# Kernel tuning notes

Hardware: AMD Instinct MI355X
Metric: run time of the kernel (lower is better)

The kernel has to match this reference:

```python
import jax, jax.numpy as jnp
import numpy as np


def _layernorm(x, g, b, eps=1e-5):
    m = x.mean(-1, keepdims=True)
    v = ((x - m) ** 2).mean(-1, keepdims=True)
    return (x - m) * jax.lax.rsqrt(v + eps) * g + b


def setup_inputs() -> dict:
    key = jax.random.key(0)
    ks = jax.random.split(key, 12)
    B, V, E, N = 8, 64, 512, 32          # batch, num_vars, embed(=input_dim), num_samples
    L, H, D, M, R = 4, 8, 64, 1024, 128  # layers, heads, head_dim, mlp_dim, resolution
    HD = H * D
    s = 0.02
    return {
        "flow_encoded": jax.random.normal(ks[0], (B, V, E), jnp.float32),
        "W_shift": s * jax.random.normal(ks[1], (E, HD), jnp.float32),
        "b_shift": jnp.zeros((HD,), jnp.float32),
        "Wk": s * jax.random.normal(ks[2], (L, H, E, D), jnp.float32),
        "bk": jnp.zeros((L, H, D), jnp.float32),
        "Wv": s * jax.random.normal(ks[3], (L, H, E, D), jnp.float32),
        "bv": jnp.zeros((L, H, D), jnp.float32),
        "ln1_g": jnp.ones((L, HD), jnp.float32),
        "ln1_b": jnp.zeros((L, HD), jnp.float32),
        "W1": s * jax.random.normal(ks[4], (L, HD, M), jnp.float32),
        "b1": jnp.zeros((L, M), jnp.float32),
        "W2": s * jax.random.normal(ks[5], (L, M, M), jnp.float32),
        "b2": jnp.zeros((L, M), jnp.float32),
        "W3": s * jax.random.normal(ks[6], (L, M, HD), jnp.float32),
        "b3": jnp.zeros((L, HD), jnp.float32),
        "ln2_g": jnp.ones((L, HD), jnp.float32),
        "ln2_b": jnp.zeros((L, HD), jnp.float32),
        "W_dist": s * jax.random.normal(ks[7], (HD, R), jnp.float32),
        "b_dist": jnp.zeros((R,), jnp.float32),
        "num_samples": N,
    }


def _forward_logits(flow_encoded, W_shift, b_shift, Wk, bk, Wv, bv,
                    ln1_g, ln1_b, W1, b1, W2, b2, W3, b3, ln2_g, ln2_b,
                    W_dist, b_dist, num_samples):
    B, V, E = flow_encoded.shape
    L, H, _, D = Wk.shape
    HD = H * D
    # history keys/values: all heads in one einsum (replaces per-head nn.Linear loop)
    keys = jnp.einsum('bve,lhed->lbhvd', flow_encoded, Wk) + bk[:, None, :, None, :]
    vals = jnp.einsum('bve,lhed->lbhvd', flow_encoded, Wv) + bv[:, None, :, None, :]
    # queries per (var, sample); vectorized over vars (outer loop in source is independent)
    att = flow_encoded @ W_shift + b_shift                      # [B, V, HD]
    att = jnp.broadcast_to(att[:, :, None, :], (B, V, num_samples, HD))
    scale = D ** -0.5
    for l in range(L):
        q = att.reshape(B, V, num_samples, H, D)
        scores = jnp.einsum('bvnhd,bhwd->bvnhw', q, keys[l]) * scale
        w = jax.nn.softmax(scores, axis=-1)
        a = jnp.einsum('bvnhw,bhwd->bvnhd', w, vals[l]).reshape(B, V, num_samples, HD)
        att = _layernorm(att + a, ln1_g[l], ln1_b[l])
        h = jax.nn.relu(att @ W1[l] + b1[l])
        h = jax.nn.relu(h @ W2[l] + b2[l])
        h = h @ W3[l] + b3[l]
        att = _layernorm(att + h, ln2_g[l], ln2_b[l])
    return att @ W_dist + b_dist                                # [B, V, N, R]


def reference(flow_encoded, W_shift, b_shift, Wk, bk, Wv, bv,
              ln1_g, ln1_b, W1, b1, W2, b2, W3, b3, ln2_g, ln2_b,
              W_dist, b_dist, num_samples):
    logits = _forward_logits(flow_encoded, W_shift, b_shift, Wk, bk, Wv, bv,
                             ln1_g, ln1_b, W1, b1, W2, b2, W3, b3, ln2_g, ln2_b,
                             W_dist, b_dist, num_samples)
    R = b_dist.shape[0]
    k = jax.random.key(1)
    idx = jax.random.categorical(jax.random.fold_in(k, 0), logits, axis=-1)  # multinomial(1)
    u = jax.random.uniform(jax.random.fold_in(k, 1), idx.shape, jnp.float32)
    samples = (idx.astype(jnp.float32) + u) / R                 # [B, V, N]
    return samples
```

## Files before the change

### kernel.cpp

```cpp
#include <hip/hip_runtime.h>
#include <hip/hip_bf16.h>
#include <math.h>

constexpr int B  = 8,  V = 64, E = 512, NS = 32;
constexpr int L  = 4,  H = 8,  D = 64,  M  = 1024, R = 128;
constexpr int HD = H * D;
constexpr int ROWS  = B * V;
constexpr int SROWS = ROWS * NS;
constexpr int KVN = 4096;

typedef _Float16 half8 __attribute__((ext_vector_type(8)));
typedef float floatx4 __attribute__((ext_vector_type(4)));

struct TF2 { unsigned a, b; };
__host__ __device__ constexpr unsigned rotl32(unsigned x, int d) {
  return (x << d) | (x >> (32 - d));
}
__host__ __device__ constexpr TF2 threefry(unsigned k0, unsigned k1,
                                           unsigned x0, unsigned x1) {
  unsigned ks2 = k0 ^ k1 ^ 0x1BD11BDAu;
  x0 += k0; x1 += k1;
  const int ra[4] = {13, 15, 26, 6};
  const int rb[4] = {17, 29, 16, 24};
  for (int i = 0; i < 4; i++) { x0 += x1; x1 = rotl32(x1, ra[i]); x1 ^= x0; }
  x0 += k1;  x1 += ks2 + 1u;
  for (int i = 0; i < 4; i++) { x0 += x1; x1 = rotl32(x1, rb[i]); x1 ^= x0; }
  x0 += ks2; x1 += k0 + 2u;
  for (int i = 0; i < 4; i++) { x0 += x1; x1 = rotl32(x1, ra[i]); x1 ^= x0; }
  x0 += k0;  x1 += k1 + 3u;
  for (int i = 0; i < 4; i++) { x0 += x1; x1 = rotl32(x1, rb[i]); x1 ^= x0; }
  x0 += k1;  x1 += ks2 + 4u;
  for (int i = 0; i < 4; i++) { x0 += x1; x1 = rotl32(x1, ra[i]); x1 ^= x0; }
  x0 += ks2; x1 += k0 + 5u;
  return {x0, x1};
}
__device__ __forceinline__ unsigned tf_bits32(unsigned k0, unsigned k1,
                                              unsigned j) {
  TF2 r = threefry(k0, k1, 0u, j);
  return r.a ^ r.b;
}

__device__ __forceinline__ double waveReduceAdd64(double v) {
#pragma unroll
  for (int m = 32; m; m >>= 1) v += __shfl_xor(v, m, 64);
  return v;
}

__device__ __forceinline__ void split16(float v, _Float16& h, _Float16& l) {
  h = (_Float16)v;
  l = (_Float16)((v - (float)h) * 2048.0f);
}

struct WArgs {
  const float* s[7];
  _Float16* h[7];
  _Float16* l[7];
};
__global__ __launch_bounds__(256) void prep_split(
    WArgs a, const float* __restrict__ flow, const float* __restrict__ bk,
    const float* __restrict__ bv, const float* __restrict__ bsh,
    _Float16* __restrict__ fh, _Float16* __restrict__ fl,
    float* __restrict__ kvb, float* __restrict__ logits) {
  __shared__ float tile[64][65];
  const int bid = blockIdx.x, t = threadIdx.x;
  if (bid < 275) {
    if (bid < 256) {
      const int base = (bid * 256 + t) * 4;
      float4 v = *(const float4*)&flow[base];
      float x[4] = {v.x, v.y, v.z, v.w};
#pragma unroll
      for (int j = 0; j < 4; j++) {
        _Float16 h, l;
        split16(x[j], h, l);
        fh[base + j] = h;
        fl[base + j] = l;
      }
    } else {
      const int idx = (bid - 256) * 256 + t;
      if (idx < KVN + HD) {
        float bb = (idx < 2048) ? bk[idx]
                 : (idx < 4096) ? bv[idx - 2048]
                                : bsh[idx - 4096];
        kvb[idx] = bb;
      }
    }
    return;
  }
  if (bid >= 2915) {
    const int idx = (bid - 2915) * 256 + t;
    float4 z = {0.f, 0.f, 0.f, 0.f};
    *(float4*)&logits[idx * 4] = z;
    return;
  }
  const int WS_OFF[8] = {0, 64, 320, 576, 1088, 2112, 2624, 2640};
  const int WS_K[7] = {512, 512, 512, 512, 1024, 1024, 512};
  const int WS_N[7] = {512, 64, 64, 1024, 1024, 512, 128};
  int wb = bid - 275;
  int mi = 0;
  while (wb >= WS_OFF[mi + 1]) mi++;
  int tt = wb - WS_OFF[mi];
  const int K = WS_K[mi], N = WS_N[mi];
  const int ktiles = K >> 6;
  const int per = ktiles * (N >> 6);
  const int z = tt / per;
  const int rem = tt - z * per;
  const int k0 = (rem % ktiles) * 64, n0 = (rem / ktiles) * 64;
  const size_t moff = (size_t)z * K * N;
  const float* src = a.s[mi] + moff;
  _Float16* dh = a.h[mi] + moff;
  _Float16* dl = a.l[mi] + moff;
#pragma unroll
  for (int i = 0; i < 16; i++) {
    int idx = i * 256 + t, r = idx >> 6, c = idx & 63;
    tile[r][c] = src[(size_t)(k0 + r) * N + n0 + c];
  }
  __syncthreads();
#pragma unroll
  for (int i = 0; i < 16; i++) {
    int idx = i * 256 + t, n = idx >> 6, k = idx & 63;
    float v = tile[k][n];
    _Float16 h, l;
    split16(v, h, l);
    dh[(size_t)(n0 + n) * K + k0 + k] = h;
    dl[(size_t)(n0 + n) * K + k0 + k] = l;
  }
}

#define GEMM64_BODY(Ah, Al, Bh, Bl, K, m0, n0, kbase, kchunk, hh, mid, lds)  \
  {                                                                          \
    const int t = threadIdx.x, lane = t & 63, wave = t >> 6;                 \
    const int KT = (kchunk) >> 5;                                            \
    const int l15w = lane & 15, quadw = lane >> 4;                           \
    const _Float16* srcs[4] = {                                              \
        (Ah) + (size_t)(m0) * (K), (Al) + (size_t)(m0) * (K),                \
        (Bh) + (size_t)(n0) * (K), (Bl) + (size_t)(n0) * (K)};               \
    const _Float16* gsrc =                                                   \
        srcs[wave] + (size_t)l15w * (K) + quadw * 8 + (kbase);               \
    auto stage = [&](int buf, int kt) {                                      \
      _Float16* base = &lds[buf * 8192 + wave * 2048];                       \
      const int koff = kt * 32;                                              \
      _Pragma("unroll") for (int f = 0; f < 4; f++)                          \
          __builtin_amdgcn_global_load_lds(                                  \
              gsrc + (size_t)(f * 16) * (K) + koff, base + f * 512, 16, 0,   \
              0);                                                            \
    };                                                                       \
    const int wm = wave >> 1, wn = wave & 1;                                 \
    stage(0, 0);                                                             \
    __syncthreads();                                                         \
    for (int kt = 0; kt < KT; kt++) {                                        \
      if (kt + 1 < KT) stage((kt + 1) & 1, kt + 1);                          \
      const int bofs = (kt & 1) * 8192;                                      \
      half8 a_h[2], a_l[2], b_h[2], b_l[2];                                  \
      _Pragma("unroll") for (int i = 0; i < 2; i++) {                        \
        const int af = (wm * 2 + i) * 512 + lane * 8;                        \
        const int bf = (wn * 2 + i) * 512 + lane * 8;                        \
        a_h[i] = *(const half8*)&lds[bofs + af];                             \
        a_l[i] = *(const half8*)&lds[bofs + 2048 + af];                      \
        b_h[i] = *(const half8*)&lds[bofs + 4096 + bf];                      \
        b_l[i] = *(const half8*)&lds[bofs + 6144 + bf];                      \
      }                                                                      \
      _Pragma("unroll") for (int i = 0; i < 2; i++)                          \
          _Pragma("unroll") for (int j = 0; j < 2; j++) {                    \
        hh[i][j] = __builtin_amdgcn_mfma_f32_16x16x32_f16(a_h[i], b_h[j],    \
                                                          hh[i][j], 0, 0, 0);\
        mid[i][j] = __builtin_amdgcn_mfma_f32_16x16x32_f16(                  \
            a_h[i], b_l[j], mid[i][j], 0, 0, 0);                             \
        mid[i][j] = __builtin_amdgcn_mfma_f32_16x16x32_f16(                  \
            a_l[i], b_h[j], mid[i][j], 0, 0, 0);                             \
      }                                                                      \
      __syncthreads();                                                       \
    }                                                                        \
  }

#define GEMM_ACC_INIT(hh, mid)                                               \
  floatx4 hh[2][2], mid[2][2];                                               \
  _Pragma("unroll") for (int i = 0; i < 2; i++)                              \
      _Pragma("unroll") for (int j = 0; j < 2; j++) {                        \
    hh[i][j] = (floatx4){0.f, 0.f, 0.f, 0.f};                                \
    mid[i][j] = (floatx4){0.f, 0.f, 0.f, 0.f};                               \
  }

__global__ __launch_bounds__(256) void gemm_kv(
    const _Float16* __restrict__ Ah, const _Float16* __restrict__ Al,
    const _Float16* __restrict__ Bh, const _Float16* __restrict__ Bl,
    const float* __restrict__ kvb, float* __restrict__ kv,
    float* __restrict__ att) {
  __shared__ __align__(16) _Float16 lds[2 * 8192];
  const int n0 = blockIdx.x * 64, m0 = blockIdx.y * 64;
  GEMM_ACC_INIT(hh, mid)
  GEMM64_BODY(Ah, Al, Bh, Bl, 512, m0, n0, 0, 512, hh, mid, lds)
  const int t = threadIdx.x, lane = t & 63, wave = t >> 6;
  const int wm = wave >> 1, wn = wave & 1, quad = lane >> 4, l15 = lane & 15;
#pragma unroll
  for (int i = 0; i < 2; i++)
#pragma unroll
    for (int j = 0; j < 2; j++)
#pragma unroll
      for (int r = 0; r < 4; r++) {
        float v = hh[i][j][r] + mid[i][j][r] * (1.0f / 2048.0f);
        const int m = m0 + (wm * 2 + i) * 16 + quad * 4 + r;
        const int n = n0 + (wn * 2 + j) * 16 + l15;
        v += kvb[n];
        if (n < KVN) kv[(size_t)m * KVN + n] = v;
        else att[(size_t)m * HD + (n - KVN)] = v;
      }
}

__global__ __launch_bounds__(256) void gemm_sp(
    const _Float16* __restrict__ Ah, const _Float16* __restrict__ Al,
    const _Float16* __restrict__ Bh, const _Float16* __restrict__ Bl,
    float* __restrict__ P, int K, int kchunk, int Ndim) {
  __shared__ __align__(16) _Float16 lds[2 * 8192];
  const int n0 = blockIdx.x * 64, m0 = blockIdx.y * 64;
  const int kbase = blockIdx.z * kchunk;
  GEMM_ACC_INIT(hh, mid)
  GEMM64_BODY(Ah, Al, Bh, Bl, K, m0, n0, kbase, kchunk, hh, mid, lds)
  const int t = threadIdx.x, lane = t & 63, wave = t >> 6;
  const int wm = wave >> 1, wn = wave & 1, quad = lane >> 4, l15 = lane & 15;
  float* Pz = P + (size_t)blockIdx.z * ROWS * Ndim;
#pragma unroll
  for (int i = 0; i < 2; i++)
#pragma unroll
    for (int j = 0; j < 2; j++)
#pragma unroll
      for (int r = 0; r < 4; r++) {
        float v = hh[i][j][r] + mid[i][j][r] * (1.0f / 2048.0f);
        const int m = m0 + (wm * 2 + i) * 16 + quad * 4 + r;
        const int n = n0 + (wn * 2 + j) * 16 + l15;
        Pz[(size_t)m * Ndim + n] = v;
      }
}

__global__ __launch_bounds__(256) void gemm_dist(
    const _Float16* __restrict__ Ah, const _Float16* __restrict__ Al,
    const _Float16* __restrict__ Bh, const _Float16* __restrict__ Bl,
    const float* __restrict__ bd, float* __restrict__ logits) {
  __shared__ __align__(16) _Float16 lds[2 * 8192];
  const int n0 = blockIdx.x * 64, m0 = blockIdx.y * 64;
  const int kbase = blockIdx.z * 256;
  GEMM_ACC_INIT(hh, mid)
  GEMM64_BODY(Ah, Al, Bh, Bl, 512, m0, n0, kbase, 256, hh, mid, lds)
  const int t = threadIdx.x, lane = t & 63, wave = t >> 6;
  const int wm = wave >> 1, wn = wave & 1, quad = lane >> 4, l15 = lane & 15;
#pragma unroll
  for (int i = 0; i < 2; i++)
#pragma unroll
    for (int j = 0; j < 2; j++)
#pragma unroll
      for (int r = 0; r < 4; r++) {
        float v = hh[i][j][r] + mid[i][j][r] * (1.0f / 2048.0f);
        const int m = m0 + (wm * 2 + i) * 16 + quad * 4 + r;
        const int n = n0 + (wn * 2 + j) * 16 + l15;
        if (blockIdx.z == 0) v += bd[n];
        atomicAdd(&logits[(size_t)m * R + n], v);
      }
}

__global__ __launch_bounds__(256) void epi_h(
    const float* __restrict__ P, const float* __restrict__ bias,
    _Float16* __restrict__ Oh, _Float16* __restrict__ Ol, int Ndim, int kz,
    int relu) {
  const int n = blockIdx.x * 256 + threadIdx.x;
  const int m = blockIdx.y;
  const size_t MN = (size_t)ROWS * Ndim;
  const size_t id = (size_t)m * Ndim + n;
  float v = 0.0f;
  for (int z = 0; z < kz; z++) v += P[z * MN + id];
  v += bias[n];
  if (relu) v = fmaxf(v, 0.0f);
  _Float16 h, l;
  split16(v, h, l);
  Oh[id] = h;
  Ol[id] = l;
}

__device__ __forceinline__ void attn_core(
    float* __restrict__ att, _Float16* __restrict__ att_h,
    _Float16* __restrict__ att_l, const float* __restrict__ kv,
    const float* __restrict__ g, const float* __restrict__ bb, int l, int row,
    float q0, float q1) {
  __shared__ float q[HD];
  __shared__ float sp[HD];
  __shared__ double rb[8];
  const int t = threadIdx.x;
  const int b_ = row >> 6;
  q[t] = q0;
  q[t + 256] = q1;
  __syncthreads();
#pragma unroll
  for (int rep = 0; rep < 2; rep++) {
    int idx = t + rep * 256;
    int h = idx >> 6, w = idx & 63;
    const float* kp = kv + (size_t)(b_ * 64 + w) * KVN + (l * 8 + h) * 64;
    const float* qp = q + h * D;
    double s = 0.0;
#pragma unroll 8
    for (int d = 0; d < 64; d++) s += (double)qp[d] * (double)kp[d];
    sp[idx] = (float)s * 0.125f;
  }
  __syncthreads();
  {
    int h = t >> 5, w0 = t & 31;
    float s0 = sp[h * 64 + w0], s1 = sp[h * 64 + w0 + 32];
    float mx = fmaxf(s0, s1);
#pragma unroll
    for (int m = 16; m; m >>= 1) mx = fmaxf(mx, __shfl_xor(mx, m, 32));
    float e0 = expf(s0 - mx), e1 = expf(s1 - mx);
    double sm = (double)e0 + (double)e1;
#pragma unroll
    for (int m = 16; m; m >>= 1) sm += __shfl_xor(sm, m, 32);
    sp[h * 64 + w0]      = (float)((double)e0 / sm);
    sp[h * 64 + w0 + 32] = (float)((double)e1 / sm);
  }
  __syncthreads();
  float x[2];
#pragma unroll
  for (int rep = 0; rep < 2; rep++) {
    int idx = t + rep * 256;
    int h = idx >> 6, d = idx & 63;
    const float* vp =
        kv + (size_t)(b_ * 64) * KVN + 2048 + (l * 8 + h) * 64 + d;
    const float* pp = sp + h * 64;
    double acc = 0.0;
#pragma unroll 8
    for (int w = 0; w < 64; w++)
      acc += (double)pp[w] * (double)vp[(size_t)w * KVN];
    x[rep] = q[idx] + (float)acc;
  }
  double s1 = (double)x[0] + (double)x[1];
  double s2 = (double)x[0] * (double)x[0] + (double)x[1] * (double)x[1];
  s1 = waveReduceAdd64(s1);
  s2 = waveReduceAdd64(s2);
  const int wid = t >> 6, lane = t & 63;
  if (lane == 0) { rb[wid] = s1; rb[4 + wid] = s2; }
  __syncthreads();
  double S1 = rb[0] + rb[1] + rb[2] + rb[3];
  double S2 = rb[4] + rb[5] + rb[6] + rb[7];
  double mean = S1 / (double)HD;
  double var  = S2 / (double)HD - mean * mean;
  double inv  = 1.0 / sqrt(var + (double)1e-5f);
  float y0 =
      (float)(((double)x[0] - mean) * inv * (double)g[t] + (double)bb[t]);
  float y1 = (float)(((double)x[1] - mean) * inv * (double)g[t + 256] +
                     (double)bb[t + 256]);
  att[row * HD + t] = y0;
  att[row * HD + 256 + t] = y1;
  _Float16 h0, l0, h1v, l1v;
  split16(y0, h0, l0);
  split16(y1, h1v, l1v);
  att_h[row * HD + t] = h0;
  att_l[row * HD + t] = l0;
  att_h[row * HD + 256 + t] = h1v;
  att_l[row * HD + 256 + t] = l1v;
}

__global__ __launch_bounds__(256) void attn_kernel(
    float* __restrict__ att, _Float16* __restrict__ att_h,
    _Float16* __restrict__ att_l, const float* __restrict__ kv,
    const float* __restrict__ g, const float* __restrict__ bb, int l) {
  const int t = threadIdx.x, row = blockIdx.x;
  float q0 = att[row * HD + t];
  float q1 = att[row * HD + 256 + t];
  attn_core(att, att_h, att_l, kv, g, bb, l, row, q0, q1);
}

__global__ __launch_bounds__(256) void epi_ln_attn(
    float* __restrict__ att, _Float16* __restrict__ att_h,
    _Float16* __restrict__ att_l, const float* __restrict__ P,
    const float* __restrict__ b3, const float* __restrict__ g2,
    const float* __restrict__ bb2, const float* __restrict__ kv,
    const float* __restrict__ g1, const float* __restrict__ bb1, int next_l) {
  __shared__ double rb[8];
  const int t = threadIdx.x, row = blockIdx.x;
  const size_t MN = (size_t)ROWS * HD;
  const size_t id0 = (size_t)row * HD + t;
  float h0 = 0.0f, h1s = 0.0f;
  for (int z = 0; z < 8; z++) {
    h0 += P[z * MN + id0];
    h1s += P[z * MN + id0 + 256];
  }
  h0 += b3[t];
  h1s += b3[t + 256];
  float x0 = att[id0] + h0;
  float x1 = att[id0 + 256] + h1s;
  double s1 = (double)x0 + (double)x1;
  double s2 = (double)x0 * (double)x0 + (double)x1 * (double)x1;
  s1 = waveReduceAdd64(s1);
  s2 = waveReduceAdd64(s2);
  const int wid = t >> 6, lane = t & 63;
  if (lane == 0) { rb[wid] = s1; rb[4 + wid] = s2; }
  __syncthreads();
  double S1 = rb[0] + rb[1] + rb[2] + rb[3];
  double S2 = rb[4] + rb[5] + rb[6] + rb[7];
  double mean = S1 / (double)HD;
  double var  = S2 / (double)HD - mean * mean;
  double inv  = 1.0 / sqrt(var + (double)1e-5f);
  float y0 =
      (float)(((double)x0 - mean) * inv * (double)g2[t] + (double)bb2[t]);
  float y1 = (float)(((double)x1 - mean) * inv * (double)g2[t + 256] +
                     (double)bb2[t + 256]);
  if (next_l < 0) {
    att[id0] = y0;
    att[id0 + 256] = y1;
    _Float16 hh0, ll0, hh1, ll1;
    split16(y0, hh0, ll0);
    split16(y1, hh1, ll1);
    att_h[id0] = hh0;
    att_l[id0] = ll0;
    att_h[id0 + 256] = hh1;
    att_l[id0 + 256] = ll1;
  } else {
    __syncthreads();
    attn_core(att, att_h, att_l, kv, g1, bb1, next_l, row, y0, y1);
  }
}

__global__ __launch_bounds__(256) void sample_kernel(
    const float* __restrict__ logits, float* __restrict__ out) {
  constexpr TF2 KC = threefry(0u, 1u, 0u, 0u);
  constexpr TF2 KU = threefry(0u, 1u, 0u, 1u);
  const int lane = threadIdx.x & 63;
  const int wid = threadIdx.x >> 6;
  const int row = blockIdx.x * 4 + wid;
  const float* lrow = logits + (row >> 5) * R;
  float bvv = -1e30f;
  int bi = 0;
#pragma unroll
  for (int rep = 0; rep < 2; rep++) {
    int r = lane + rep * 64;
    unsigned j = (unsigned)row * (unsigned)R + (unsigned)r;
    unsigned bits = tf_bits32(KC.a, KC.b, j);
    float f = __uint_as_float((bits >> 9) | 0x3f800000u) - 1.0f;
    float u = fmaxf(f, 1.17549435e-38f);
    float gv = -logf(-logf(u));
    float v = lrow[r] + gv;
    if (v > bvv) { bvv = v; bi = r; }
  }
#pragma unroll
  for (int m = 32; m; m >>= 1) {
    float ov = __shfl_xor(bvv, m, 64);
    int oi = __shfl_xor(bi, m, 64);
    if (ov > bvv || (ov == bvv && oi < bi)) { bvv = ov; bi = oi; }
  }
  if (lane == 0) {
    unsigned ub = tf_bits32(KU.a, KU.b, (unsigned)row);
    float u = __uint_as_float((ub >> 9) | 0x3f800000u) - 1.0f;
    out[row] = ((float)bi + u) * (1.0f / 128.0f);
  }
}

extern "C" void kernel_launch(void* const* d_in, const int* in_sizes, int n_in,
                              void* d_out, int out_size, void* d_ws,
                              size_t ws_size, hipStream_t stream) {
  (void)in_sizes; (void)n_in; (void)out_size; (void)ws_size;
  const float* flow = (const float*)d_in[0];
  const float* Wsh  = (const float*)d_in[1];
  const float* bsh  = (const float*)d_in[2];
  const float* Wk   = (const float*)d_in[3];
  const float* bk   = (const float*)d_in[4];
  const float* Wv   = (const float*)d_in[5];
  const float* bv   = (const float*)d_in[6];
  const float* ln1g = (const float*)d_in[7];
  const float* ln1b = (const float*)d_in[8];
  const float* W1   = (const float*)d_in[9];
  const float* b1   = (const float*)d_in[10];
  const float* W2   = (const float*)d_in[11];
  const float* b2   = (const float*)d_in[12];
  const float* W3   = (const float*)d_in[13];
  const float* b3   = (const float*)d_in[14];
  const float* ln2g = (const float*)d_in[15];
  const float* ln2b = (const float*)d_in[16];
  const float* Wd   = (const float*)d_in[17];
  const float* bd   = (const float*)d_in[18];

  float* ws = (float*)d_ws;
  float* kv     = ws;
  float* att    = kv + ROWS * KVN;
  float* logits = att + ROWS * HD;
  float* kvb    = logits + ROWS * R;
  float* P      = kvb + 4608;
  _Float16* hp = (_Float16*)(P + 4718592);
  _Float16* flow_h = hp;            hp += 262144;
  _Float16* flow_l = hp;            hp += 262144;
  _Float16* BKV_h  = hp;            hp += 4608 * 512;
  _Float16* BKV_l  = hp;            hp += 4608 * 512;
  _Float16* W1_h   = hp;            hp += 2097152;
  _Float16* W1_l   = hp;            hp += 2097152;
  _Float16* W2_h   = hp;            hp += 4194304;
  _Float16* W2_l   = hp;            hp += 4194304;
  _Float16* W3_h   = hp;            hp += 2097152;
  _Float16* W3_l   = hp;            hp += 2097152;
  _Float16* Wd_h   = hp;            hp += 65536;
  _Float16* Wd_l   = hp;            hp += 65536;
  _Float16* att_h  = hp;            hp += 262144;
  _Float16* att_l  = hp;            hp += 262144;
  _Float16* h1_h   = hp;            hp += 524288;
  _Float16* h1_l   = hp;            hp += 524288;
  _Float16* h2_h   = hp;            hp += 524288;
  _Float16* h2_l   = hp;            hp += 524288;

  WArgs wa;
  wa.s[0] = Wsh; wa.h[0] = BKV_h + 4096 * 512; wa.l[0] = BKV_l + 4096 * 512;
  wa.s[1] = Wk;  wa.h[1] = BKV_h;              wa.l[1] = BKV_l;
  wa.s[2] = Wv;  wa.h[2] = BKV_h + 2048 * 512; wa.l[2] = BKV_l + 2048 * 512;
  wa.s[3] = W1;  wa.h[3] = W1_h;  wa.l[3] = W1_l;
  wa.s[4] = W2;  wa.h[4] = W2_h;  wa.l[4] = W2_l;
  wa.s[5] = W3;  wa.h[5] = W3_h;  wa.l[5] = W3_l;
  wa.s[6] = Wd;  wa.h[6] = Wd_h;  wa.l[6] = Wd_l;
  prep_split<<<2979, 256, 0, stream>>>(wa, flow, bk, bv, bsh, flow_h, flow_l,
                                       kvb, logits);

  gemm_kv<<<dim3(72, 8), 256, 0, stream>>>(flow_h, flow_l, BKV_h, BKV_l, kvb,
                                           kv, att);
  attn_kernel<<<ROWS, 256, 0, stream>>>(att, att_h, att_l, kv, ln1g, ln1b, 0);

  for (int l = 0; l < L; l++) {
    gemm_sp<<<dim3(16, 8, 4), 256, 0, stream>>>(
        att_h, att_l, W1_h + (size_t)l * 524288, W1_l + (size_t)l * 524288, P,
        512, 128, M);
    epi_h<<<dim3(4, ROWS), 256, 0, stream>>>(P, b1 + l * M, h1_h, h1_l, M, 4,
                                             1);
    gemm_sp<<<dim3(16, 8, 8), 256, 0, stream>>>(
        h1_h, h1_l, W2_h + (size_t)l * 1048576, W2_l + (size_t)l * 1048576, P,
        1024, 128, M);
    epi_h<<<dim3(4, ROWS), 256, 0, stream>>>(P, b2 + l * M, h2_h, h2_l, M, 8,
                                             1);
    gemm_sp<<<dim3(8, 8, 8), 256, 0, stream>>>(
        h2_h, h2_l, W3_h + (size_t)l * 524288, W3_l + (size_t)l * 524288, P,
        1024, 128, HD);
    const int nl = (l + 1 < L) ? (l + 1) : -1;
    epi_ln_attn<<<ROWS, 256, 0, stream>>>(
        att, att_h, att_l, P, b3 + l * HD, ln2g + l * HD, ln2b + l * HD, kv,
        ln1g + (nl < 0 ? 0 : nl) * HD, ln1b + (nl < 0 ? 0 : nl) * HD, nl);
  }
  gemm_dist<<<dim3(2, 8, 2), 256, 0, stream>>>(att_h, att_l, Wd_h, Wd_l, bd,
                                               logits);
  sample_kernel<<<SROWS / 4, 256, 0, stream>>>(logits, (float*)d_out);
}
```

Before: 419.5 us.

## Drop split-K for MLP GEMMs and fuse bias/ReLU/split epilogue into GEMM

Replaces the split-K GEMM plus separate epi_h reduction kernels for W1 and W2 with a single full-K GEMM that applies bias, ReLU and the fp16 hi/lo split in its epilogue. It also halves the split-K factor for W3 and removes split-K and atomics from the final distribution GEMM, which makes the logits zeroing in prep_split unnecessary. This cuts kernel launches and the partial-sum round trips through global memory. In exchange the W1/W2 grids shrink to 128 blocks with long K loops, which leaves much of the GPU idle.

Result: slower. 459.6 us (+9.6%).

```diff
diff --git a/kernel.cpp b/kernel.cpp
--- a/kernel.cpp
+++ b/kernel.cpp
@@ -60,7 +60,7 @@
     WArgs a, const float* __restrict__ flow, const float* __restrict__ bk,
     const float* __restrict__ bv, const float* __restrict__ bsh,
     _Float16* __restrict__ fh, _Float16* __restrict__ fl,
-    float* __restrict__ kvb, float* __restrict__ logits) {
+    float* __restrict__ kvb) {
   __shared__ float tile[64][65];
   const int bid = blockIdx.x, t = threadIdx.x;
   if (bid < 275) {
@@ -84,12 +84,6 @@
         kvb[idx] = bb;
       }
     }
-    return;
-  }
-  if (bid >= 2915) {
-    const int idx = (bid - 2915) * 256 + t;
-    float4 z = {0.f, 0.f, 0.f, 0.f};
-    *(float4*)&logits[idx * 4] = z;
     return;
   }
   const int WS_OFF[8] = {0, 64, 320, 576, 1088, 2112, 2624, 2640};
@@ -231,15 +225,44 @@
       }
 }
 
+__global__ __launch_bounds__(256) void gemm_eh(
+    const _Float16* __restrict__ Ah, const _Float16* __restrict__ Al,
+    const _Float16* __restrict__ Bh, const _Float16* __restrict__ Bl,
+    const float* __restrict__ bias, _Float16* __restrict__ Oh,
+    _Float16* __restrict__ Ol, int K, int Ndim, int relu) {
+  __shared__ __align__(16) _Float16 lds[2 * 8192];
+  const int n0 = blockIdx.x * 64, m0 = blockIdx.y * 64;
+  GEMM_ACC_INIT(hh, mid)
+  GEMM64_BODY(Ah, Al, Bh, Bl, K, m0, n0, 0, K, hh, mid, lds)
+  const int t = threadIdx.x, lane = t & 63, wave = t >> 6;
+  const int wm = wave >> 1, wn = wave & 1, quad = lane >> 4, l15 = lane & 15;
+#pragma unroll
+  for (int i = 0; i < 2; i++)
+#pragma unroll
+    for (int j = 0; j < 2; j++)
+#pragma unroll
+      for (int r = 0; r < 4; r++) {
+        float v = hh[i][j][r] + mid[i][j][r] * (1.0f / 2048.0f);
+        const int m = m0 + (wm * 2 + i) * 16 + quad * 4 + r;
+        const int n = n0 + (wn * 2 + j) * 16 + l15;
+        v += bias[n];
+        if (relu) v = fmaxf(v, 0.0f);
+        _Float16 h, l;
+        split16(v, h, l);
+        const size_t id = (size_t)m * Ndim + n;
+        Oh[id] = h;
+        Ol[id] = l;
+      }
+}
+
 __global__ __launch_bounds__(256) void gemm_dist(
     const _Float16* __restrict__ Ah, const _Float16* __restrict__ Al,
     const _Float16* __restrict__ Bh, const _Float16* __restrict__ Bl,
     const float* __restrict__ bd, float* __restrict__ logits) {
   __shared__ __align__(16) _Float16 lds[2 * 8192];
   const int n0 = blockIdx.x * 64, m0 = blockIdx.y * 64;
-  const int kbase = blockIdx.z * 256;
   GEMM_ACC_INIT(hh, mid)
-  GEMM64_BODY(Ah, Al, Bh, Bl, 512, m0, n0, kbase, 256, hh, mid, lds)
+  GEMM64_BODY(Ah, Al, Bh, Bl, 512, m0, n0, 0, 512, hh, mid, lds)
   const int t = threadIdx.x, lane = t & 63, wave = t >> 6;
   const int wm = wave >> 1, wn = wave & 1, quad = lane >> 4, l15 = lane & 15;
 #pragma unroll
@@ -251,27 +274,8 @@
         float v = hh[i][j][r] + mid[i][j][r] * (1.0f / 2048.0f);
         const int m = m0 + (wm * 2 + i) * 16 + quad * 4 + r;
         const int n = n0 + (wn * 2 + j) * 16 + l15;
-        if (blockIdx.z == 0) v += bd[n];
-        atomicAdd(&logits[(size_t)m * R + n], v);
+        logits[(size_t)m * R + n] = v + bd[n];
       }
-}
-
-__global__ __launch_bounds__(256) void epi_h(
-    const float* __restrict__ P, const float* __restrict__ bias,
-    _Float16* __restrict__ Oh, _Float16* __restrict__ Ol, int Ndim, int kz,
-    int relu) {
-  const int n = blockIdx.x * 256 + threadIdx.x;
-  const int m = blockIdx.y;
-  const size_t MN = (size_t)ROWS * Ndim;
-  const size_t id = (size_t)m * Ndim + n;
-  float v = 0.0f;
-  for (int z = 0; z < kz; z++) v += P[z * MN + id];
-  v += bias[n];
-  if (relu) v = fmaxf(v, 0.0f);
-  _Float16 h, l;
-  split16(v, h, l);
-  Oh[id] = h;
-  Ol[id] = l;
 }
 
 __device__ __forceinline__ void attn_core(
@@ -369,13 +373,14 @@
     _Float16* __restrict__ att_l, const float* __restrict__ P,
     const float* __restrict__ b3, const float* __restrict__ g2,
     const float* __restrict__ bb2, const float* __restrict__ kv,
-    const float* __restrict__ g1, const float* __restrict__ bb1, int next_l) {
+    const float* __restrict__ g1, const float* __restrict__ bb1, int next_l,
+    int kz) {
   __shared__ double rb[8];
   const int t = threadIdx.x, row = blockIdx.x;
   const size_t MN = (size_t)ROWS * HD;
   const size_t id0 = (size_t)row * HD + t;
   float h0 = 0.0f, h1s = 0.0f;
-  for (int z = 0; z < 8; z++) {
+  for (int z = 0; z < kz; z++) {
     h0 += P[z * MN + id0];
     h1s += P[z * MN + id0 + 256];
   }
@@ -507,33 +512,29 @@
   wa.s[4] = W2;  wa.h[4] = W2_h;  wa.l[4] = W2_l;
   wa.s[5] = W3;  wa.h[5] = W3_h;  wa.l[5] = W3_l;
   wa.s[6] = Wd;  wa.h[6] = Wd_h;  wa.l[6] = Wd_l;
-  prep_split<<<2979, 256, 0, stream>>>(wa, flow, bk, bv, bsh, flow_h, flow_l,
-                                       kvb, logits);
+  prep_split<<<2915, 256, 0, stream>>>(wa, flow, bk, bv, bsh, flow_h, flow_l,
+                                       kvb);
 
   gemm_kv<<<dim3(72, 8), 256, 0, stream>>>(flow_h, flow_l, BKV_h, BKV_l, kvb,
                                            kv, att);
   attn_kernel<<<ROWS, 256, 0, stream>>>(att, att_h, att_l, kv, ln1g, ln1b, 0);
 
   for (int l = 0; l < L; l++) {
-    gemm_sp<<<dim3(16, 8, 4), 256, 0, stream>>>(
-        att_h, att_l, W1_h + (size_t)l * 524288, W1_l + (size_t)l * 524288, P,
-        512, 128, M);
-    epi_h<<<dim3(4, ROWS), 256, 0, stream>>>(P, b1 + l * M, h1_h, h1_l, M, 4,
-                                             1);
-    gemm_sp<<<dim3(16, 8, 8), 256, 0, stream>>>(
-        h1_h, h1_l, W2_h + (size_t)l * 1048576, W2_l + (size_t)l * 1048576, P,
-        1024, 128, M);
-    epi_h<<<dim3(4, ROWS), 256, 0, stream>>>(P, b2 + l * M, h2_h, h2_l, M, 8,
-                                             1);
-    gemm_sp<<<dim3(8, 8, 8), 256, 0, stream>>>(
+    gemm_eh<<<dim3(16, 8), 256, 0, stream>>>(
+        att_h, att_l, W1_h + (size_t)l * 524288, W1_l + (size_t)l * 524288,
+        b1 + l * M, h1_h, h1_l, 512, M, 1);
+    gemm_eh<<<dim3(16, 8), 256, 0, stream>>>(
+        h1_h, h1_l, W2_h + (size_t)l * 1048576, W2_l + (size_t)l * 1048576,
+        b2 + l * M, h2_h, h2_l, 1024, M, 1);
+    gemm_sp<<<dim3(8, 8, 4), 256, 0, stream>>>(
         h2_h, h2_l, W3_h + (size_t)l * 524288, W3_l + (size_t)l * 524288, P,
-        1024, 128, HD);
+        1024, 256, HD);
     const int nl = (l + 1 < L) ? (l + 1) : -1;
     epi_ln_attn<<<ROWS, 256, 0, stream>>>(
         att, att_h, att_l, P, b3 + l * HD, ln2g + l * HD, ln2b + l * HD, kv,
-        ln1g + (nl < 0 ? 0 : nl) * HD, ln1b + (nl < 0 ? 0 : nl) * HD, nl);
-  }
-  gemm_dist<<<dim3(2, 8, 2), 256, 0, stream>>>(att_h, att_l, Wd_h, Wd_l, bd,
-                                               logits);
+        ln1g + (nl < 0 ? 0 : nl) * HD, ln1b + (nl < 0 ? 0 : nl) * HD, nl, 4);
+  }
+  gemm_dist<<<dim3(2, 8), 256, 0, stream>>>(att_h, att_l, Wd_h, Wd_l, bd,
+                                            logits);
   sample_kernel<<<SROWS / 4, 256, 0, stream>>>(logits, (float*)d_out);
 }
```
